# Kernel tuning notes

Hardware: AMD Instinct MI355X
Metric: run time of the kernel (lower is better)

## Reference

```python
import jax, jax.numpy as jnp
import numpy as np

D_MODEL = 1024
N_HEADS = 16
HEAD_DIM = D_MODEL // N_HEADS


def setup_inputs() -> dict:
    key = jax.random.key(0)
    ks = jax.random.split(key, 9)
    B, S = 2, 2048
    s = 1.0 / np.sqrt(D_MODEL)
    x = jax.random.normal(ks[0], (B, S, D_MODEL), dtype=jnp.float32)
    Wq = jax.random.normal(ks[1], (N_HEADS, D_MODEL, HEAD_DIM), dtype=jnp.float32) * s
    Wk = jax.random.normal(ks[2], (N_HEADS, D_MODEL, HEAD_DIM), dtype=jnp.float32) * s
    Wv = jax.random.normal(ks[3], (N_HEADS, D_MODEL, HEAD_DIM), dtype=jnp.float32) * s
    bq = jax.random.normal(ks[4], (N_HEADS, HEAD_DIM), dtype=jnp.float32) * s
    bk = jax.random.normal(ks[5], (N_HEADS, HEAD_DIM), dtype=jnp.float32) * s
    bv = jax.random.normal(ks[6], (N_HEADS, HEAD_DIM), dtype=jnp.float32) * s
    Wp = jax.random.normal(ks[7], (D_MODEL, D_MODEL), dtype=jnp.float32) * s
    bp = jax.random.normal(ks[8], (D_MODEL,), dtype=jnp.float32) * s
    return {"x": x, "Wq": Wq, "Wk": Wk, "Wv": Wv, "bq": bq, "bk": bk, "bv": bv, "Wp": Wp, "bp": bp}


def reference(x, Wq, Wk, Wv, bq, bk, bv, Wp, bp):
    # Per-head projections batched over heads: [B,S,D] x [H,D,E] -> [B,H,S,E]
    Q = jnp.einsum('bsd,hde->bhse', x, Wq) + bq[None, :, None, :]
    K = jnp.einsum('bsd,hde->bhse', x, Wk) + bk[None, :, None, :]
    V = jnp.einsum('bsd,hde->bhse', x, Wv) + bv[None, :, None, :]
    scores = jnp.einsum('bhse,bhte->bhst', Q, K) / jnp.sqrt(jnp.asarray(HEAD_DIM, x.dtype))
    attn = jax.nn.softmax(scores, axis=-1)          # [B,H,S,S]
    out = jnp.einsum('bhst,bhte->bhse', attn, V)    # [B,H,S,E]
    B, H, S, E = out.shape
    concat = out.transpose(0, 2, 1, 3).reshape(B, S, H * E)  # concat heads along feature
    return concat @ Wp.T + bp
```

## Files before the change

### kernel.cpp

```cpp
#include <hip/hip_runtime.h>
#include <hip/hip_bf16.h>

typedef __attribute__((ext_vector_type(8))) short short8;
typedef __attribute__((ext_vector_type(4))) short svec4;
typedef __attribute__((ext_vector_type(4))) float float4_t;
typedef __attribute__((ext_vector_type(8))) _Float16 half8;

#define D_MODEL 1024
#define N_HEADS 16
#define HEAD_DIM 64
#define B_SZ 2
#define SEQ 2048
#define M_ROWS (B_SZ*SEQ)
#define NQKV 3072
#define SC_LOG2E 0.18033688011112042f

__device__ __forceinline__ unsigned short f2bf(float f) {
  unsigned u = __float_as_uint(f);
  u += 0x7FFFu + ((u >> 16) & 1u);
  return (unsigned short)(u >> 16);
}

__device__ __forceinline__ unsigned short f2h(float f) {
  _Float16 h = (_Float16)f;
  return *(unsigned short*)&h;
}

__device__ __forceinline__ void gl_lds16(const unsigned short* g, unsigned short* l) {
  __builtin_amdgcn_global_load_lds(
      (const __attribute__((address_space(1))) unsigned int*)(size_t)g,
      (__attribute__((address_space(3))) unsigned int*)(unsigned int)(size_t)l,
      16, 0, 0);
}

__global__ void prep(const float* __restrict__ x, const float* __restrict__ Wp,
                     const float* __restrict__ Wq, const float* __restrict__ Wk,
                     const float* __restrict__ Wv,
                     unsigned short* __restrict__ xb, unsigned short* __restrict__ Wpb,
                     unsigned short* __restrict__ Wall) {
  __shared__ float ts[64][65];
  int bid = blockIdx.x;
  if (bid < 5120) {
    const float* src; unsigned short* dst; int base;
    if (bid < 4096) { src = x;  dst = xb;  base = bid * 1024 + threadIdx.x * 4; }
    else            { src = Wp; dst = Wpb; base = (bid - 4096) * 1024 + threadIdx.x * 4; }
    float4 v = *(const float4*)(src + base);
    dst[base + 0] = f2bf(v.x);
    dst[base + 1] = f2bf(v.y);
    dst[base + 2] = f2bf(v.z);
    dst[base + 3] = f2bf(v.w);
  } else {
    int u = bid - 5120;
    int sel = u >> 8;
    int rem = u & 255;
    int hh = rem >> 4, dt = rem & 15;
    int d0 = dt * 64;
    const float* W = sel == 0 ? Wq : (sel == 1 ? Wk : Wv);
    int ldr = threadIdx.x >> 2, ec = (threadIdx.x & 3) * 16;
    const float* src = W + (size_t)hh * (D_MODEL * HEAD_DIM) + (size_t)(d0 + ldr) * HEAD_DIM + ec;
#pragma unroll
    for (int j = 0; j < 4; j++) {
      float4 v = *(const float4*)(src + j * 4);
      ts[ldr][ec + j * 4 + 0] = v.x;
      ts[ldr][ec + j * 4 + 1] = v.y;
      ts[ldr][ec + j * 4 + 2] = v.z;
      ts[ldr][ec + j * 4 + 3] = v.w;
    }
    __syncthreads();
    int er = threadIdx.x >> 2, dc = (threadIdx.x & 3) * 16;
    short8 o0, o1;
#pragma unroll
    for (int j = 0; j < 8; j++) {
      o0[j] = (short)f2bf(ts[dc + j][er]);
      o1[j] = (short)f2bf(ts[dc + 8 + j][er]);
    }
    unsigned short* dst = Wall + (size_t)(sel * 1024 + hh * 64 + er) * D_MODEL + d0 + dc;
    *(short8*)dst = o0;
    *(short8*)(dst + 8) = o1;
  }
}

__global__ __launch_bounds__(256) void qkv_gemm(const unsigned short* __restrict__ xb,
                                                const unsigned short* __restrict__ Wall,
                                                const float* __restrict__ bq,
                                                const float* __restrict__ bk,
                                                const float* __restrict__ bv,
                                                unsigned short* __restrict__ Qb,
                                                unsigned short* __restrict__ Kb,
                                                unsigned short* __restrict__ Vtb) {
  __shared__ unsigned short As[128 * 64], Bs[128 * 64];
  __shared__ __align__(16) unsigned short Stage[4][16 * 72];
  const int m0 = blockIdx.x * 128, n0 = blockIdx.y * 128;
  const int lane = threadIdx.x & 63, w = threadIdx.x >> 6;
  const int l16 = lane & 15, quad = lane >> 4;
  const int wm = w & 1, wn = w >> 1;
  const int sr = lane >> 3;
  const int scol = ((lane & 7) ^ sr) * 8;
  const unsigned short* gaA = xb + (size_t)(m0 + w * 32 + sr) * D_MODEL + scol;
  const unsigned short* gaB = Wall + (size_t)(n0 + w * 32 + sr) * D_MODEL + scol;
  unsigned short* lA = As + (w * 32) * 64;
  unsigned short* lB = Bs + (w * 32) * 64;
  const int rswz = (l16 & 7);
  float4_t acc[4][4];
  float4_t z = {0.f, 0.f, 0.f, 0.f};
#pragma unroll
  for (int i = 0; i < 4; i++)
#pragma unroll
    for (int j = 0; j < 4; j++) acc[i][j] = z;
  for (int k0 = 0; k0 < D_MODEL; k0 += 64) {
    __syncthreads();
#pragma unroll
    for (int j = 0; j < 4; j++) {
      gl_lds16(gaA + (size_t)j * 8 * D_MODEL + k0, lA + j * 8 * 64);
      gl_lds16(gaB + (size_t)j * 8 * D_MODEL + k0, lB + j * 8 * 64);
    }
    __syncthreads();
#pragma unroll
    for (int kk = 0; kk < 2; kk++) {
      const int ch = ((kk * 4 + quad) ^ rswz) * 8;
      short8 af[4], bf[4];
#pragma unroll
      for (int i = 0; i < 4; i++)
        af[i] = *(const short8*)&As[(wm * 64 + i * 16 + l16) * 64 + ch];
#pragma unroll
      for (int j = 0; j < 4; j++)
        bf[j] = *(const short8*)&Bs[(wn * 64 + j * 16 + l16) * 64 + ch];
#pragma unroll
      for (int i = 0; i < 4; i++)
#pragma unroll
        for (int j = 0; j < 4; j++)
          acc[i][j] = __builtin_amdgcn_mfma_f32_16x16x32_bf16(af[i], bf[j], acc[i][j], 0, 0, 0);
    }
  }
  const int nb = n0 + wn * 64;
  const int sel = nb >> 10;
  const int h = (nb >> 6) & 15;
  const float* bias = sel == 0 ? bq : (sel == 1 ? bk : bv);
  const int mbase = m0 + wm * 64;
  const int bb = mbase >> 11;
  const size_t bh = (size_t)(bb * N_HEADS + h);
  if (sel == 2) {
    unsigned short* vs = &Stage[w][0];
    const size_t vbase = bh * (32 * 4096) + (size_t)((mbase >> 6) & 31) * 4096;
    const int e8 = lane >> 3, ch2 = lane & 7;
#pragma unroll
    for (int j = 0; j < 4; j++) {
      float be = bias[h * 64 + j * 16 + l16];
#pragma unroll
      for (int i = 0; i < 4; i++)
#pragma unroll
        for (int r = 0; r < 4; r++)
          vs[l16 * 72 + i * 16 + quad * 4 + r] = f2h(acc[i][j][r] + be);
#pragma unroll
      for (int rd = 0; rd < 2; rd++) {
        int er = rd * 8 + e8;
        short8 val = *(const short8*)(vs + er * 72 + ch2 * 8);
        *(short8*)(Vtb + vbase + (size_t)(j * 16 + er) * 64 + ch2 * 8) = val;
      }
    }
  } else {
    unsigned short* st = &Stage[w][0];
    unsigned short* dst = (sel == 0) ? Qb : Kb;
    const float qsc = (sel == 0) ? SC_LOG2E : 1.0f;
    const size_t rowbase = bh * SEQ + (mbase & (SEQ - 1));
    const int r2 = lane >> 1, c2 = lane & 1;
#pragma unroll
    for (int j = 0; j < 4; j++) {
      float be = bias[h * 64 + j * 16 + l16];
#pragma unroll
      for (int i = 0; i < 4; i++)
#pragma unroll
        for (int r = 0; r < 4; r++)
          st[(i * 16 + quad * 4 + r) * 18 + l16] = f2bf((acc[i][j][r] + be) * qsc);
#pragma unroll
      for (int p = 0; p < 2; p++) {
        int row = p * 32 + r2;
        short8 val = *(const short8*)(st + row * 18 + c2 * 8);
        *(short8*)(dst + (rowbase + row) * HEAD_DIM + j * 16 + c2 * 8) = val;
      }
    }
  }
}

__global__ __launch_bounds__(512) void attn_kernel(const unsigned short* __restrict__ Q,
                                                   const unsigned short* __restrict__ K,
                                                   const unsigned short* __restrict__ Vt,
                                                   unsigned short* __restrict__ concat) {
  __shared__ __align__(16) union ShU {
    unsigned short kv[2][4][64 * 64];
    struct { float4_t ot[4][4][4][16][4]; float ls[4][4][16]; } c;
  } sh;
  const int lin = blockIdx.x;
  const int xcd = lin & 7, slot = lin >> 3;
  const int bh_i = xcd * 4 + (slot >> 3);
  const int b = bh_i >> 4, h = bh_i & 15;
  const int qt = slot & 7;
  const int tid = threadIdx.x;
  const int lane = tid & 63, w = tid >> 6;
  const int g = w >> 2, wq = w & 3;
  const int l16 = lane & 15, quad = lane >> 4;
  const size_t bh = (size_t)bh_i;
  const int q0 = qt * 256 + wq * 64;
  const int tb = g * 1024;
  float4_t z = {0.f, 0.f, 0.f, 0.f};

  short8 aq[4][2];
#pragma unroll
  for (int rg = 0; rg < 4; rg++)
#pragma unroll
    for (int hf = 0; hf < 2; hf++)
      aq[rg][hf] = *(const short8*)(Q + (bh * SEQ + q0 + rg * 16 + l16) * HEAD_DIM + hf * 32 + quad * 8);

  const int tl = tid & 255;
  const int krow = tl >> 2, kch = (tl & 3) * 8;
  const unsigned short* kg = K + (bh * SEQ + tb + krow) * HEAD_DIM + kch;
  const int swz = (krow & 7) << 3;
  const int ktw0 = (krow * 64 + kch) ^ swz;
  const int ktw1 = (krow * 64 + kch + 32) ^ swz;
  const int vt0 = (tl & 3) * 16, vt1 = vt0 + 8;
  const unsigned short* vg = Vt + bh * (32 * 4096) + (size_t)(tb >> 6) * 4096 + krow * 64 + vt0;
  const int tp0 = ((vt0 >> 5) << 5) + (((vt0 >> 2) & 3) << 3) + (((vt0 >> 4) & 1) << 2);
  const int tp1 = ((vt1 >> 5) << 5) + (((vt1 >> 2) & 3) << 3) + (((vt1 >> 4) & 1) << 2);
  const int vtwA = (krow * 64 + tp0) ^ swz;
  const int vtwB = (krow * 64 + tp0 + 8) ^ swz;
  const int vtwC = (krow * 64 + tp1) ^ swz;
  const int vtwD = (krow * 64 + tp1 + 8) ^ swz;
  const int rsw = (l16 & 7) << 3;

  float4_t o[4][4];
#pragma unroll
  for (int rg = 0; rg < 4; rg++)
#pragma unroll
    for (int ne = 0; ne < 4; ne++) o[rg][ne] = z;
  float lsp[4] = {0.f, 0.f, 0.f, 0.f};

  short8 kreg0 = *(const short8*)kg;
  short8 kreg1 = *(const short8*)(kg + 32);
  short8 vreg0 = *(const short8*)vg;
  short8 vreg1 = *(const short8*)(vg + 8);
  kg += 4096; vg += 4096;

  auto step = [&](unsigned short* kb, unsigned short* vb, int itv) {
    *(short8*)(kb + ktw0) = kreg0;
    *(short8*)(kb + ktw1) = kreg1;
    svec4 a0 = {vreg0[0], vreg0[1], vreg0[2], vreg0[3]};
    svec4 a1 = {vreg0[4], vreg0[5], vreg0[6], vreg0[7]};
    svec4 b0 = {vreg1[0], vreg1[1], vreg1[2], vreg1[3]};
    svec4 b1 = {vreg1[4], vreg1[5], vreg1[6], vreg1[7]};
    *(svec4*)(vb + vtwA) = a0;
    *(svec4*)(vb + vtwB) = a1;
    *(svec4*)(vb + vtwC) = b0;
    *(svec4*)(vb + vtwD) = b1;
    __syncthreads();
    if (itv < 15) {
      kreg0 = *(const short8*)kg;
      kreg1 = *(const short8*)(kg + 32);
      vreg0 = *(const short8*)vg;
      vreg1 = *(const short8*)(vg + 8);
      kg += 4096; vg += 4096;
    }
#pragma unroll
    for (int p = 0; p < 2; p++) {
      float4_t s[2][4];
      __builtin_amdgcn_s_setprio(1);
#pragma unroll
      for (int tcl = 0; tcl < 2; tcl++) {
        int tc = 2 * p + tcl;
        short8 kf0 = *(const short8*)(kb + (((tc * 16 + l16) * 64 + quad * 8) ^ rsw));
        short8 kf1 = *(const short8*)(kb + (((tc * 16 + l16) * 64 + quad * 8 + 32) ^ rsw));
#pragma unroll
        for (int rg = 0; rg < 4; rg++) {
          s[tcl][rg] = __builtin_amdgcn_mfma_f32_16x16x32_bf16(kf0, aq[rg][0], z, 0, 0, 0);
          s[tcl][rg] = __builtin_amdgcn_mfma_f32_16x16x32_bf16(kf1, aq[rg][1], s[tcl][rg], 0, 0, 0);
        }
      }
      __builtin_amdgcn_s_setprio(0);
      half8 vf[4];
#pragma unroll
      for (int ne = 0; ne < 4; ne++)
        vf[ne] = *(const half8*)(vb + (((ne * 16 + l16) * 64 + p * 32 + quad * 8) ^ rsw));
#pragma unroll
      for (int rg = 0; rg < 4; rg++) {
        float pv[8];
#pragma unroll
        for (int r = 0; r < 4; r++) {
          pv[r]     = __builtin_amdgcn_exp2f(s[0][rg][r]);
          pv[4 + r] = __builtin_amdgcn_exp2f(s[1][rg][r]);
        }
        lsp[rg] += ((pv[0] + pv[1]) + (pv[2] + pv[3])) + ((pv[4] + pv[5]) + (pv[6] + pv[7]));
        half8 pa = {(_Float16)pv[0], (_Float16)pv[1], (_Float16)pv[2], (_Float16)pv[3],
                    (_Float16)pv[4], (_Float16)pv[5], (_Float16)pv[6], (_Float16)pv[7]};
        __builtin_amdgcn_s_setprio(1);
#pragma unroll
        for (int ne = 0; ne < 4; ne++)
          o[rg][ne] = __builtin_amdgcn_mfma_f32_16x16x32_f16(pa, vf[ne], o[rg][ne], 0, 0, 0);
        __builtin_amdgcn_s_setprio(0);
      }
    }
  };

  for (int it2 = 0; it2 < 8; ++it2) {
    step(sh.kv[g][0], sh.kv[g][2], 2 * it2);
    step(sh.kv[g][1], sh.kv[g][3], 2 * it2 + 1);
  }

  float lsf[4];
#pragma unroll
  for (int rg = 0; rg < 4; rg++) {
    float v = lsp[rg];
    v += __shfl_xor(v, 16, 64);
    v += __shfl_xor(v, 32, 64);
    lsf[rg] = v;
  }

  __syncthreads();
  if (g) {
#pragma unroll
    for (int rg = 0; rg < 4; rg++) {
#pragma unroll
      for (int ne = 0; ne < 4; ne++) sh.c.ot[wq][rg][ne][l16][quad] = o[rg][ne];
      if (quad == 0) sh.c.ls[wq][rg][l16] = lsf[rg];
    }
  }
  __syncthreads();
  if (!g) {
#pragma unroll
    for (int rg = 0; rg < 4; rg++) {
      float lt = lsf[rg] + sh.c.ls[wq][rg][l16];
#pragma unroll
      for (int ne = 0; ne < 4; ne++) {
        float4_t pp = sh.c.ot[wq][rg][ne][l16][quad];
        o[rg][ne] += pp;
      }
#pragma unroll
      for (int r = 0; r < 4; r++) {
        float li = 1.0f / __shfl(lt, quad * 4 + r, 64);
        int sr2 = q0 + rg * 16 + quad * 4 + r;
#pragma unroll
        for (int ne = 0; ne < 4; ne++)
          concat[((size_t)(b * SEQ + sr2)) * D_MODEL + h * 64 + ne * 16 + l16] = f2bf(o[rg][ne][r] * li);
      }
    }
  }
}

__global__ __launch_bounds__(256) void out_gemm(const unsigned short* __restrict__ cb,
                                                const unsigned short* __restrict__ Wpb,
                                                const float* __restrict__ bp,
                                                float* __restrict__ out) {
  __shared__ unsigned short As[128 * 64], Bs[128 * 64];
  const int m0 = blockIdx.x * 128, n0 = blockIdx.y * 128;
  const int lane = threadIdx.x & 63, w = threadIdx.x >> 6;
  const int l16 = lane & 15, quad = lane >> 4;
  const int wm = w & 1, wn = w >> 1;
  const int sr = lane >> 3;
  const int scol = ((lane & 7) ^ sr) * 8;
  const unsigned short* gaA = cb + (size_t)(m0 + w * 32 + sr) * D_MODEL + scol;
  const unsigned short* gaB = Wpb + (size_t)(n0 + w * 32 + sr) * D_MODEL + scol;
  unsigned short* lA = As + (w * 32) * 64;
  unsigned short* lB = Bs + (w * 32) * 64;
  const int rswz = (l16 & 7);
  float4_t acc[4][4];
  float4_t z = {0.f, 0.f, 0.f, 0.f};
#pragma unroll
  for (int i = 0; i < 4; i++)
#pragma unroll
    for (int j = 0; j < 4; j++) acc[i][j] = z;
  for (int k0 = 0; k0 < D_MODEL; k0 += 64) {
    __syncthreads();
#pragma unroll
    for (int j = 0; j < 4; j++) {
      gl_lds16(gaA + (size_t)j * 8 * D_MODEL + k0, lA + j * 8 * 64);
      gl_lds16(gaB + (size_t)j * 8 * D_MODEL + k0, lB + j * 8 * 64);
    }
    __syncthreads();
#pragma unroll
    for (int kk = 0; kk < 2; kk++) {
      const int ch = ((kk * 4 + quad) ^ rswz) * 8;
      short8 af[4], bf[4];
#pragma unroll
      for (int i = 0; i < 4; i++)
        af[i] = *(const short8*)&As[(wm * 64 + i * 16 + l16) * 64 + ch];
#pragma unroll
      for (int j = 0; j < 4; j++)
        bf[j] = *(const short8*)&Bs[(wn * 64 + j * 16 + l16) * 64 + ch];
#pragma unroll
      for (int i = 0; i < 4; i++)
#pragma unroll
        for (int j = 0; j < 4; j++)
          acc[i][j] = __builtin_amdgcn_mfma_f32_16x16x32_bf16(af[i], bf[j], acc[i][j], 0, 0, 0);
    }
  }
#pragma unroll
  for (int i = 0; i < 4; i++)
#pragma unroll
    for (int j = 0; j < 4; j++)
#pragma unroll
      for (int r = 0; r < 4; r++) {
        int m = m0 + wm * 64 + i * 16 + quad * 4 + r;
        int oc = n0 + wn * 64 + j * 16 + l16;
        out[(size_t)m * D_MODEL + oc] = acc[i][j][r] + bp[oc];
      }
}

extern "C" void kernel_launch(void* const* d_in, const int* in_sizes, int n_in,
                              void* d_out, int out_size, void* d_ws, size_t ws_size,
                              hipStream_t stream) {
  const float* x  = (const float*)d_in[0];
  const float* Wq = (const float*)d_in[1];
  const float* Wk = (const float*)d_in[2];
  const float* Wv = (const float*)d_in[3];
  const float* bq = (const float*)d_in[4];
  const float* bk = (const float*)d_in[5];
  const float* bv = (const float*)d_in[6];
  const float* Wp = (const float*)d_in[7];
  const float* bp = (const float*)d_in[8];
  float* out = (float*)d_out;

  char* ws = (char*)d_ws;
  size_t off = 0;
  auto alloc = [&](size_t bytes) -> void* {
    void* p = ws + off;
    off += (bytes + 255) & ~(size_t)255;
    return p;
  };
  unsigned short* xb   = (unsigned short*)alloc((size_t)M_ROWS * D_MODEL * 2);
  unsigned short* Wall = (unsigned short*)alloc((size_t)NQKV * D_MODEL * 2);
  unsigned short* Wpb  = (unsigned short*)alloc((size_t)D_MODEL * D_MODEL * 2);
  unsigned short* Qb   = (unsigned short*)alloc((size_t)B_SZ * N_HEADS * SEQ * HEAD_DIM * 2);
  unsigned short* Kb   = (unsigned short*)alloc((size_t)B_SZ * N_HEADS * SEQ * HEAD_DIM * 2);
  unsigned short* Vtb  = (unsigned short*)alloc((size_t)B_SZ * N_HEADS * SEQ * HEAD_DIM * 2);
  unsigned short* cbuf = (unsigned short*)alloc((size_t)B_SZ * SEQ * D_MODEL * 2);

  prep<<<5888, 256, 0, stream>>>(x, Wp, Wq, Wk, Wv, xb, Wpb, Wall);

  qkv_gemm<<<dim3(M_ROWS / 128, NQKV / 128), 256, 0, stream>>>(xb, Wall, bq, bk, bv, Qb, Kb, Vtb);

  attn_kernel<<<256, 512, 0, stream>>>(Qb, Kb, Vtb, cbuf);

  out_gemm<<<dim3(M_ROWS / 128, D_MODEL / 128), 256, 0, stream>>>(cbuf, Wpb, bp, out);
}
```

Baseline: 185.5 us.

## Double-buffer LDS tiles in QKV and output projection GEMMs

Both projection GEMMs now use two LDS buffers per operand and issue the next K-tile's global-to-LDS loads before computing on the current tile. The two barriers per iteration become one. This is meant to hide global load latency behind MFMA work. It doubles LDS usage per block, which may lower occupancy.

```diff
diff --git a/kernel.cpp b/kernel.cpp
--- a/kernel.cpp
+++ b/kernel.cpp
@@ -88,7 +88,7 @@
                                                 unsigned short* __restrict__ Qb,
                                                 unsigned short* __restrict__ Kb,
                                                 unsigned short* __restrict__ Vtb) {
-  __shared__ unsigned short As[128 * 64], Bs[128 * 64];
+  __shared__ unsigned short As[2][128 * 64], Bs[2][128 * 64];
   __shared__ __align__(16) unsigned short Stage[4][16 * 72];
   const int m0 = blockIdx.x * 128, n0 = blockIdx.y * 128;
   const int lane = threadIdx.x & 63, w = threadIdx.x >> 6;
@@ -98,8 +98,6 @@
   const int scol = ((lane & 7) ^ sr) * 8;
   const unsigned short* gaA = xb + (size_t)(m0 + w * 32 + sr) * D_MODEL + scol;
   const unsigned short* gaB = Wall + (size_t)(n0 + w * 32 + sr) * D_MODEL + scol;
-  unsigned short* lA = As + (w * 32) * 64;
-  unsigned short* lB = Bs + (w * 32) * 64;
   const int rswz = (l16 & 7);
   float4_t acc[4][4];
   float4_t z = {0.f, 0.f, 0.f, 0.f};
@@ -107,30 +105,38 @@
   for (int i = 0; i < 4; i++)
 #pragma unroll
     for (int j = 0; j < 4; j++) acc[i][j] = z;
-  for (int k0 = 0; k0 < D_MODEL; k0 += 64) {
-    __syncthreads();
+
+  auto stage = [&](int buf, int k0) {
 #pragma unroll
     for (int j = 0; j < 4; j++) {
-      gl_lds16(gaA + (size_t)j * 8 * D_MODEL + k0, lA + j * 8 * 64);
-      gl_lds16(gaB + (size_t)j * 8 * D_MODEL + k0, lB + j * 8 * 64);
-    }
-    __syncthreads();
+      gl_lds16(gaA + (size_t)j * 8 * D_MODEL + k0, &As[buf][(w * 32 + j * 8) * 64]);
+      gl_lds16(gaB + (size_t)j * 8 * D_MODEL + k0, &Bs[buf][(w * 32 + j * 8) * 64]);
+    }
+  };
+
+  stage(0, 0);
+  __syncthreads();
+  int cur = 0;
+  for (int t = 0; t < 16; ++t) {
+    if (t < 15) stage(cur ^ 1, (t + 1) * 64);
 #pragma unroll
     for (int kk = 0; kk < 2; kk++) {
       const int ch = ((kk * 4 + quad) ^ rswz) * 8;
       short8 af[4], bf[4];
 #pragma unroll
       for (int i = 0; i < 4; i++)
-        af[i] = *(const short8*)&As[(wm * 64 + i * 16 + l16) * 64 + ch];
+        af[i] = *(const short8*)&As[cur][(wm * 64 + i * 16 + l16) * 64 + ch];
 #pragma unroll
       for (int j = 0; j < 4; j++)
-        bf[j] = *(const short8*)&Bs[(wn * 64 + j * 16 + l16) * 64 + ch];
+        bf[j] = *(const short8*)&Bs[cur][(wn * 64 + j * 16 + l16) * 64 + ch];
 #pragma unroll
       for (int i = 0; i < 4; i++)
 #pragma unroll
         for (int j = 0; j < 4; j++)
           acc[i][j] = __builtin_amdgcn_mfma_f32_16x16x32_bf16(af[i], bf[j], acc[i][j], 0, 0, 0);
     }
+    __syncthreads();
+    cur ^= 1;
   }
   const int nb = n0 + wn * 64;
   const int sel = nb >> 10;
@@ -348,7 +354,7 @@
                                                 const unsigned short* __restrict__ Wpb,
                                                 const float* __restrict__ bp,
                                                 float* __restrict__ out) {
-  __shared__ unsigned short As[128 * 64], Bs[128 * 64];
+  __shared__ unsigned short As[2][128 * 64], Bs[2][128 * 64];
   const int m0 = blockIdx.x * 128, n0 = blockIdx.y * 128;
   const int lane = threadIdx.x & 63, w = threadIdx.x >> 6;
   const int l16 = lane & 15, quad = lane >> 4;
@@ -357,8 +363,6 @@
   const int scol = ((lane & 7) ^ sr) * 8;
   const unsigned short* gaA = cb + (size_t)(m0 + w * 32 + sr) * D_MODEL + scol;
   const unsigned short* gaB = Wpb + (size_t)(n0 + w * 32 + sr) * D_MODEL + scol;
-  unsigned short* lA = As + (w * 32) * 64;
-  unsigned short* lB = Bs + (w * 32) * 64;
   const int rswz = (l16 & 7);
   float4_t acc[4][4];
   float4_t z = {0.f, 0.f, 0.f, 0.f};
@@ -366,30 +370,38 @@
   for (int i = 0; i < 4; i++)
 #pragma unroll
     for (int j = 0; j < 4; j++) acc[i][j] = z;
-  for (int k0 = 0; k0 < D_MODEL; k0 += 64) {
-    __syncthreads();
+
+  auto stage = [&](int buf, int k0) {
 #pragma unroll
     for (int j = 0; j < 4; j++) {
-      gl_lds16(gaA + (size_t)j * 8 * D_MODEL + k0, lA + j * 8 * 64);
-      gl_lds16(gaB + (size_t)j * 8 * D_MODEL + k0, lB + j * 8 * 64);
-    }
-    __syncthreads();
+      gl_lds16(gaA + (size_t)j * 8 * D_MODEL + k0, &As[buf][(w * 32 + j * 8) * 64]);
+      gl_lds16(gaB + (size_t)j * 8 * D_MODEL + k0, &Bs[buf][(w * 32 + j * 8) * 64]);
+    }
+  };
+
+  stage(0, 0);
+  __syncthreads();
+  int cur = 0;
+  for (int t = 0; t < 16; ++t) {
+    if (t < 15) stage(cur ^ 1, (t + 1) * 64);
 #pragma unroll
     for (int kk = 0; kk < 2; kk++) {
       const int ch = ((kk * 4 + quad) ^ rswz) * 8;
       short8 af[4], bf[4];
 #pragma unroll
       for (int i = 0; i < 4; i++)
-        af[i] = *(const short8*)&As[(wm * 64 + i * 16 + l16) * 64 + ch];
+        af[i] = *(const short8*)&As[cur][(wm * 64 + i * 16 + l16) * 64 + ch];
 #pragma unroll
       for (int j = 0; j < 4; j++)
-        bf[j] = *(const short8*)&Bs[(wn * 64 + j * 16 + l16) * 64 + ch];
+        bf[j] = *(const short8*)&Bs[cur][(wn * 64 + j * 16 + l16) * 64 + ch];
 #pragma unroll
       for (int i = 0; i < 4; i++)
 #pragma unroll
         for (int j = 0; j < 4; j++)
           acc[i][j] = __builtin_amdgcn_mfma_f32_16x16x32_bf16(af[i], bf[j], acc[i][j], 0, 0, 0);
     }
+    __syncthreads();
+    cur ^= 1;
   }
 #pragma unroll
   for (int i = 0; i < 4; i++)
```

New measurement: 182.2 us. No clear change (-1.8%).
